# Optimization experiments

Measured on AMD Instinct MI355X. Metric: run time of the kernel, lower is better.

Reference implementation:

```python
import jax, jax.numpy as jnp
import numpy as np


def setup_inputs() -> dict:
    key = jax.random.key(0)
    k1, k2, k3 = jax.random.split(key, 3)
    d_model, L, batch = 1024, 8192, 2
    h = jax.random.normal(k1, (d_model, L), dtype=jnp.float32)
    x = jax.random.normal(k2, (batch, d_model, L), dtype=jnp.float32)
    B = jax.random.normal(k3, (d_model, 1), dtype=jnp.float32)
    return {"h": h, "x": x, "B": B}


def reference(h, x, B):
    # L = max(x.shape[-1], h.shape[-1]); static under jit
    L = max(x.shape[-1], h.shape[-1])
    n = 2 * L  # zero-pad to 2L for linear (non-circular) convolution
    # torch norm='forward': rfft scaled by 1/n, irfft unscaled
    h_f = jnp.fft.rfft(h, n=n, norm="forward")          # (d, L+1) complex
    x_f = jnp.fft.rfft(x, n=n)                            # (b, d, L+1) complex
    y = jnp.fft.irfft(h_f * x_f, n=n, norm="forward")[..., :L]
    y = y + x * B  # residual with per-channel gate, B broadcasts over L
    return y.astype(h.dtype)
```

## Files before the change

### kernel.cpp

```cpp
#include <hip/hip_runtime.h>


#define L_SEQ   8192
#define N_FFT   16384
#define D_MODEL 1024
#define NTH     1024

#define SWZ(i) ((i) ^ (((i) >> 4) & 15))

#define C16_1 0.92387953251128675613f
#define S16_1 0.38268343236508977173f
#define C16_2 0.70710678118654752440f

__device__ __forceinline__ float2 cmul(float2 a, float2 b) {
    return make_float2(a.x * b.x - a.y * b.y, a.x * b.y + a.y * b.x);
}

__device__ __forceinline__ float2 hw_cis(float rev) {
    return make_float2(__builtin_amdgcn_cosf(rev), __builtin_amdgcn_sinf(rev));
}

__device__ __forceinline__ unsigned bf2pack(float re, float im) {
    unsigned br = __float_as_uint(re);
    br = (br + 0x7fffu + ((br >> 16) & 1u)) >> 16;
    unsigned bi = __float_as_uint(im);
    bi = (bi + 0x7fffu + ((bi >> 16) & 1u)) & 0xffff0000u;
    return br | bi;
}

__device__ __forceinline__ unsigned bf2pack2(float2 v) { return bf2pack(v.x, v.y); }

__device__ __forceinline__ float2 bf2unpack(unsigned p) {
    return make_float2(__uint_as_float(p << 16), __uint_as_float(p & 0xffff0000u));
}

template <int S>
__device__ __forceinline__ void bfly4(float2& r0, float2& r1, float2& r2, float2& r3) {
    const float2 t0 = make_float2(r0.x + r2.x, r0.y + r2.y);
    const float2 t1 = make_float2(r0.x - r2.x, r0.y - r2.y);
    const float2 t2 = make_float2(r1.x + r3.x, r1.y + r3.y);
    const float2 t3 = make_float2(r1.x - r3.x, r1.y - r3.y);
    r0 = make_float2(t0.x + t2.x, t0.y + t2.y);
    r2 = make_float2(t0.x - t2.x, t0.y - t2.y);
    if (S < 0) {
        r1 = make_float2(t1.x + t3.y, t1.y - t3.x);
        r3 = make_float2(t1.x - t3.y, t1.y + t3.x);
    } else {
        r1 = make_float2(t1.x - t3.y, t1.y + t3.x);
        r3 = make_float2(t1.x + t3.y, t1.y - t3.x);
    }
}

__device__ __forceinline__ float2 cmulc(float2 a, float re, float im) {
    return make_float2(a.x * re - a.y * im, a.x * im + a.y * re);
}

template <int S>
__device__ __forceinline__ void dft16_mid_twiddle(float2 a[16]) {
    const float s = (float)S;
    a[5]  = cmulc(a[5],   C16_1,  s * S16_1);
    a[9]  = cmulc(a[9],   C16_2,  s * C16_2);
    a[13] = cmulc(a[13],  S16_1,  s * C16_1);
    a[6]  = cmulc(a[6],   C16_2,  s * C16_2);
    a[10] = make_float2(-s * a[10].y, s * a[10].x);
    a[14] = cmulc(a[14], -C16_2,  s * C16_2);
    a[7]  = cmulc(a[7],   S16_1,  s * C16_1);
    a[11] = cmulc(a[11], -C16_2,  s * C16_2);
    a[15] = cmulc(a[15], -C16_1, -s * S16_1);
}

template <int S>
__device__ __forceinline__ void dft16(float2 a[16]) {
    bfly4<S>(a[0], a[4], a[8],  a[12]);
    bfly4<S>(a[1], a[5], a[9],  a[13]);
    bfly4<S>(a[2], a[6], a[10], a[14]);
    bfly4<S>(a[3], a[7], a[11], a[15]);
    dft16_mid_twiddle<S>(a);
    bfly4<S>(a[0],  a[1],  a[2],  a[3]);
    bfly4<S>(a[4],  a[5],  a[6],  a[7]);
    bfly4<S>(a[8],  a[9],  a[10], a[11]);
    bfly4<S>(a[12], a[13], a[14], a[15]);
}

template <int S>
__device__ __forceinline__ void inner4_halfzero(float2 a[16]) {
#pragma unroll
    for (int c = 0; c < 4; ++c) {
        const float2 p = a[c], q = a[c + 4];
        a[c]      = make_float2(p.x + q.x, p.y + q.y);
        a[c + 8]  = make_float2(p.x - q.x, p.y - q.y);
        if (S < 0) {
            a[c + 4]  = make_float2(p.x + q.y, p.y - q.x);
            a[c + 12] = make_float2(p.x - q.y, p.y + q.x);
        } else {
            a[c + 4]  = make_float2(p.x - q.y, p.y + q.x);
            a[c + 12] = make_float2(p.x + q.y, p.y - q.x);
        }
    }
}

__device__ __forceinline__ void fwd_stage1_finish(unsigned* __restrict__ zz,
                                                  const int tid, float2 a[16]) {
    dft16_mid_twiddle<-1>(a);
    bfly4<-1>(a[0],  a[1],  a[2],  a[3]);
    bfly4<-1>(a[4],  a[5],  a[6],  a[7]);
    bfly4<-1>(a[8],  a[9],  a[10], a[11]);
    bfly4<-1>(a[12], a[13], a[14], a[15]);
    const float2 w1 = hw_cis(-(float)tid * (1.0f / 16384.0f));
    zz[SWZ(tid)] = bf2pack2(a[0]);
    float2 wc = w1;
#pragma unroll
    for (int L = 1; L < 16; ++L) {
        const int P = ((L & 3) << 2) | (L >> 2);
        zz[SWZ(tid + (L << 10))] = bf2pack2(cmul(a[P], wc));
        wc = cmul(wc, w1);
    }
    __syncthreads();
}

template <int S, int LQ>
__device__ __forceinline__ void fft16_stage_bf(unsigned* __restrict__ zz, const int tid) {
    const int q = 1 << LQ;
    const int j = tid & (q - 1);
    const int base = ((tid >> LQ) << (LQ + 4)) | j;
    const float2 w1 = hw_cis((float)S * (float)j / (float)(1 << (LQ + 4)));
    float2 a[16];
    if (S < 0) {
#pragma unroll
        for (int m = 0; m < 16; ++m) a[m] = bf2unpack(zz[SWZ(base + m * q)]);
        dft16<S>(a);
        zz[SWZ(base)] = bf2pack2(a[0]);
        float2 wc = w1;
#pragma unroll
        for (int L = 1; L < 16; ++L) {
            const int P = ((L & 3) << 2) | (L >> 2);
            zz[SWZ(base + L * q)] = bf2pack2(cmul(a[P], wc));
            wc = cmul(wc, w1);
        }
    } else {
#pragma unroll
        for (int k = 0; k < 16; ++k) a[k] = bf2unpack(zz[SWZ(base + k * q)]);
        float2 wc = w1;
#pragma unroll
        for (int k = 1; k < 16; ++k) { a[k] = cmul(a[k], wc); wc = cmul(wc, w1); }
        dft16<S>(a);
#pragma unroll
        for (int M = 0; M < 16; ++M) {
            const int P = ((M & 3) << 2) | (M >> 2);
            zz[SWZ(base + M * q)] = bf2pack2(a[P]);
        }
    }
    __syncthreads();
}

__global__ void __launch_bounds__(NTH) fftconv_filter_kernel(
        const float* __restrict__ h, const float* __restrict__ Bg,
        unsigned* __restrict__ Hws) {
    extern __shared__ unsigned zz[];
    const int d = blockIdx.x;
    const int tid = threadIdx.x;
    const float invn = 1.0f / (float)N_FFT;
    const float Bs = Bg[d] * invn;

    {
        const float* hrow = h + (size_t)d * L_SEQ;
        float2 a[16];
#pragma unroll
        for (int m = 0; m < 8; ++m)
            a[m] = make_float2(hrow[tid + (m << 10)], 0.0f);
        inner4_halfzero<-1>(a);
        fwd_stage1_finish(zz, tid, a);
    }
    fft16_stage_bf<-1, 6>(zz, tid);
    fft16_stage_bf<-1, 2>(zz, tid);

    unsigned* Hrow = Hws + (size_t)d * N_FFT;
#pragma unroll
    for (int r = 0; r < 4; ++r) {
        const int i = tid + r * NTH;
        const int b = 4 * i;
        float2 a0 = bf2unpack(zz[SWZ(b)]);
        float2 a1 = bf2unpack(zz[SWZ(b + 1)]);
        float2 a2 = bf2unpack(zz[SWZ(b + 2)]);
        float2 a3 = bf2unpack(zz[SWZ(b + 3)]);
        bfly4<-1>(a0, a1, a2, a3);
        ((uint4*)(Hrow + b))[0] = make_uint4(
            bf2pack(a0.x * invn + Bs, a0.y * invn),
            bf2pack(a1.x * invn + Bs, a1.y * invn),
            bf2pack(a2.x * invn + Bs, a2.y * invn),
            bf2pack(a3.x * invn + Bs, a3.y * invn));
    }
}

__global__ void __launch_bounds__(NTH) fftconv_conv_kernel(
        const float* __restrict__ x, const unsigned* __restrict__ Hws,
        float* __restrict__ y) {
    extern __shared__ unsigned zz[];
    const int d = blockIdx.x;
    const int tid = threadIdx.x;

    const float* x0 = x + (size_t)d * L_SEQ;
    const float* x1 = x + (size_t)(D_MODEL + d) * L_SEQ;

    {
        float2 a[16];
#pragma unroll
        for (int m = 0; m < 8; ++m) {
            const int idx = tid + (m << 10);
            a[m] = make_float2(x0[idx], x1[idx]);
        }
        inner4_halfzero<-1>(a);
        fwd_stage1_finish(zz, tid, a);
    }
    fft16_stage_bf<-1, 6>(zz, tid);

    const uint4* Hp = (const uint4*)(Hws + (size_t)d * N_FFT);
    const uint4 hp0 = Hp[tid];
    const uint4 hp1 = Hp[tid + NTH];
    const uint4 hp2 = Hp[tid + 2 * NTH];
    const uint4 hp3 = Hp[tid + 3 * NTH];

    fft16_stage_bf<-1, 2>(zz, tid);

#pragma unroll
    for (int r = 0; r < 4; ++r) {
        const int b = 4 * (tid + r * NTH);
        const int p0 = SWZ(b), p1 = SWZ(b + 1), p2 = SWZ(b + 2), p3 = SWZ(b + 3);
        float2 a0 = bf2unpack(zz[p0]);
        float2 a1 = bf2unpack(zz[p1]);
        float2 a2 = bf2unpack(zz[p2]);
        float2 a3 = bf2unpack(zz[p3]);
        bfly4<-1>(a0, a1, a2, a3);
        const uint4 hp = (r == 0) ? hp0 : (r == 1) ? hp1 : (r == 2) ? hp2 : hp3;
        a0 = cmul(a0, bf2unpack(hp.x));
        a1 = cmul(a1, bf2unpack(hp.y));
        a2 = cmul(a2, bf2unpack(hp.z));
        a3 = cmul(a3, bf2unpack(hp.w));
        bfly4<+1>(a0, a1, a2, a3);
        zz[p0] = bf2pack2(a0);
        zz[p1] = bf2pack2(a1);
        zz[p2] = bf2pack2(a2);
        zz[p3] = bf2pack2(a3);
    }
    __syncthreads();

    fft16_stage_bf<+1, 2>(zz, tid);
    fft16_stage_bf<+1, 6>(zz, tid);

    {
        float2 a[16];
#pragma unroll
        for (int k = 0; k < 16; ++k) a[k] = bf2unpack(zz[SWZ(tid + (k << 10))]);
        const float2 w1 = hw_cis((float)tid * (1.0f / 16384.0f));
        float2 wc = w1;
#pragma unroll
        for (int k = 1; k < 16; ++k) { a[k] = cmul(a[k], wc); wc = cmul(wc, w1); }
        bfly4<+1>(a[0], a[4], a[8],  a[12]);
        bfly4<+1>(a[1], a[5], a[9],  a[13]);
        bfly4<+1>(a[2], a[6], a[10], a[14]);
        bfly4<+1>(a[3], a[7], a[11], a[15]);
        dft16_mid_twiddle<+1>(a);
        float* y0 = y + (size_t)d * L_SEQ;
        float* y1 = y + (size_t)(D_MODEL + d) * L_SEQ;
#pragma unroll
        for (int g = 0; g < 4; ++g) {
            const float2 b0 = a[4*g], b1 = a[4*g+1], b2 = a[4*g+2], b3 = a[4*g+3];
            const float2 t0 = make_float2(b0.x + b2.x, b0.y + b2.y);
            const float2 t1 = make_float2(b0.x - b2.x, b0.y - b2.y);
            const float2 t2 = make_float2(b1.x + b3.x, b1.y + b3.y);
            const float2 t3 = make_float2(b1.x - b3.x, b1.y - b3.y);
            const float2 r0 = make_float2(t0.x + t2.x, t0.y + t2.y);
            const float2 r1 = make_float2(t1.x - t3.y, t1.y + t3.x);
            const int q0 = tid + (g << 10);
            const int q1 = tid + ((g + 4) << 10);
            y0[q0] = r0.x; y1[q0] = r0.y;
            y0[q1] = r1.x; y1[q1] = r1.y;
        }
    }
}

extern "C" void kernel_launch(void* const* d_in, const int* in_sizes, int n_in,
                              void* d_out, int out_size, void* d_ws, size_t ws_size,
                              hipStream_t stream) {
    const float* h = (const float*)d_in[0];
    const float* x = (const float*)d_in[1];
    const float* B = (const float*)d_in[2];
    float* y = (float*)d_out;
    unsigned* Hws = (unsigned*)d_ws;

    const size_t lds_bytes = (size_t)N_FFT * sizeof(unsigned);

    fftconv_filter_kernel<<<dim3(D_MODEL), dim3(NTH), lds_bytes, stream>>>(h, B, Hws);
    fftconv_conv_kernel<<<dim3(D_MODEL), dim3(NTH), lds_bytes, stream>>>(x, Hws, y);
}
```

Measured before the change: 104.3 us.

## Replace block barriers with wave-local fences in wave-contained FFT stages

Drops the __syncthreads at the end of each radix-16 stage. Where a stage's data stays within one wavefront, it now uses a wave-level LDS wait plus a scheduling barrier instead. The final radix-4 and the pointwise-multiply pass are remapped so each wave works on its own contiguous region of the shared buffer, which keeps those stages wave-local. The filter-spectrum global loads are issued earlier, before the first stage, so their latency overlaps more compute. This only stays correct if every stage's access pattern really is wave-contained, and it relies on the cross-wave stages still having a full barrier.

Result: no change. 104.4 us (+0.1%).

```diff
diff --git a/kernel.cpp b/kernel.cpp
--- a/kernel.cpp
+++ b/kernel.cpp
@@ -12,8 +12,16 @@
 #define S16_1 0.38268343236508977173f
 #define C16_2 0.70710678118654752440f
 
+__device__ __forceinline__ void wave_fence() {
+    asm volatile("s_waitcnt lgkmcnt(0)" ::: "memory");
+    __builtin_amdgcn_sched_barrier(0);
+}
+
 __device__ __forceinline__ float2 cmul(float2 a, float2 b) {
     return make_float2(a.x * b.x - a.y * b.y, a.x * b.y + a.y * b.x);
+}
+__device__ __forceinline__ float2 cmulc(float2 a, float re, float im) {
+    return make_float2(a.x * re - a.y * im, a.x * im + a.y * re);
 }
 
 __device__ __forceinline__ float2 hw_cis(float rev) {
@@ -27,7 +35,6 @@
     bi = (bi + 0x7fffu + ((bi >> 16) & 1u)) & 0xffff0000u;
     return br | bi;
 }
-
 __device__ __forceinline__ unsigned bf2pack2(float2 v) { return bf2pack(v.x, v.y); }
 
 __device__ __forceinline__ float2 bf2unpack(unsigned p) {
@@ -51,10 +58,6 @@
     }
 }
 
-__device__ __forceinline__ float2 cmulc(float2 a, float re, float im) {
-    return make_float2(a.x * re - a.y * im, a.x * im + a.y * re);
-}
-
 template <int S>
 __device__ __forceinline__ void dft16_mid_twiddle(float2 a[16]) {
     const float s = (float)S;
@@ -150,7 +153,6 @@
             zz[SWZ(base + M * q)] = bf2pack2(a[P]);
         }
     }
-    __syncthreads();
 }
 
 __global__ void __launch_bounds__(NTH) fftconv_filter_kernel(
@@ -159,6 +161,7 @@
     extern __shared__ unsigned zz[];
     const int d = blockIdx.x;
     const int tid = threadIdx.x;
+    const int w = tid >> 6, l = tid & 63;
     const float invn = 1.0f / (float)N_FFT;
     const float Bs = Bg[d] * invn;
 
@@ -172,19 +175,21 @@
         fwd_stage1_finish(zz, tid, a);
     }
     fft16_stage_bf<-1, 6>(zz, tid);
+    wave_fence();
     fft16_stage_bf<-1, 2>(zz, tid);
+    wave_fence();
 
     unsigned* Hrow = Hws + (size_t)d * N_FFT;
 #pragma unroll
     for (int r = 0; r < 4; ++r) {
-        const int i = tid + r * NTH;
-        const int b = 4 * i;
+        const int qi = (w << 8) + (r << 6) + l;
+        const int b = qi << 2;
         float2 a0 = bf2unpack(zz[SWZ(b)]);
         float2 a1 = bf2unpack(zz[SWZ(b + 1)]);
         float2 a2 = bf2unpack(zz[SWZ(b + 2)]);
         float2 a3 = bf2unpack(zz[SWZ(b + 3)]);
         bfly4<-1>(a0, a1, a2, a3);
-        ((uint4*)(Hrow + b))[0] = make_uint4(
+        ((uint4*)Hrow)[qi] = make_uint4(
             bf2pack(a0.x * invn + Bs, a0.y * invn),
             bf2pack(a1.x * invn + Bs, a1.y * invn),
             bf2pack(a2.x * invn + Bs, a2.y * invn),
@@ -198,6 +203,7 @@
     extern __shared__ unsigned zz[];
     const int d = blockIdx.x;
     const int tid = threadIdx.x;
+    const int w = tid >> 6, l = tid & 63;
 
     const float* x0 = x + (size_t)d * L_SEQ;
     const float* x1 = x + (size_t)(D_MODEL + d) * L_SEQ;
@@ -212,19 +218,22 @@
         inner4_halfzero<-1>(a);
         fwd_stage1_finish(zz, tid, a);
     }
+
+    const uint4* Hp = (const uint4*)(Hws + (size_t)d * N_FFT);
+    const int qbase = (w << 8) + l;
+    const uint4 hp0 = Hp[qbase];
+    const uint4 hp1 = Hp[qbase + 64];
+    const uint4 hp2 = Hp[qbase + 128];
+    const uint4 hp3 = Hp[qbase + 192];
+
     fft16_stage_bf<-1, 6>(zz, tid);
-
-    const uint4* Hp = (const uint4*)(Hws + (size_t)d * N_FFT);
-    const uint4 hp0 = Hp[tid];
-    const uint4 hp1 = Hp[tid + NTH];
-    const uint4 hp2 = Hp[tid + 2 * NTH];
-    const uint4 hp3 = Hp[tid + 3 * NTH];
-
+    wave_fence();
     fft16_stage_bf<-1, 2>(zz, tid);
+    wave_fence();
 
 #pragma unroll
     for (int r = 0; r < 4; ++r) {
-        const int b = 4 * (tid + r * NTH);
+        const int b = ((w << 8) + (r << 6) + l) << 2;
         const int p0 = SWZ(b), p1 = SWZ(b + 1), p2 = SWZ(b + 2), p3 = SWZ(b + 3);
         float2 a0 = bf2unpack(zz[p0]);
         float2 a1 = bf2unpack(zz[p1]);
@@ -242,10 +251,12 @@
         zz[p2] = bf2pack2(a2);
         zz[p3] = bf2pack2(a3);
     }
+    wave_fence();
+
+    fft16_stage_bf<+1, 2>(zz, tid);
+    wave_fence();
+    fft16_stage_bf<+1, 6>(zz, tid);
     __syncthreads();
-
-    fft16_stage_bf<+1, 2>(zz, tid);
-    fft16_stage_bf<+1, 6>(zz, tid);
 
     {
         float2 a[16];
```
